# Performance work log

Measured on AMD Instinct MI355X. Metric: run time of the kernel, lower is better.

The kernel has to match this reference:

```python
import jax, jax.numpy as jnp
import numpy as np


def setup_inputs() -> dict:
    key = jax.random.key(0)
    x = jax.random.normal(key, (4096, 512), dtype=jnp.float32)
    return {"x": x}


def reference(x):
    # Pairwise Euclidean distances for all (i, j) with i > j, flattened in the
    # same order as the original nested loop: (1,0),(2,0),(2,1),(3,0),...
    n = x.shape[0]
    sq = jnp.sum(x * x, axis=1)                      # [N]
    gram = x @ x.T                                   # [N, N]
    d2 = sq[:, None] + sq[None, :] - 2.0 * gram      # [N, N] squared dists
    ii, jj = jnp.tril_indices(n, k=-1)               # row-major lower triangle
    return jnp.sqrt(jnp.maximum(d2[ii, jj], 0.0))    # [N*(N-1)/2]
```

## Files before the change

kernel.cpp:

```cpp
#include <hip/hip_runtime.h>
#include <hip/hip_bf16.h>
#include <stdint.h>

#define N 4096
#define D 512
#define TILE 128
#define BK 128
#define KITERS (D / BK)
#define NB (N / TILE)

typedef float f32x4 __attribute__((ext_vector_type(4)));
typedef int   i32x8 __attribute__((ext_vector_type(8)));
typedef int   i32x4 __attribute__((ext_vector_type(4)));

__global__ __launch_bounds__(256) void prep_kernel(const float* __restrict__ x,
                                                   unsigned char* __restrict__ xq,
                                                   float* __restrict__ sq) {
    int row  = blockIdx.x * 4 + (threadIdx.x >> 6);
    int lane = threadIdx.x & 63;
    const float* xr = x + (size_t)row * D + lane * 8;
    float4 v0 = *reinterpret_cast<const float4*>(xr);
    float4 v1 = *reinterpret_cast<const float4*>(xr + 4);

    int w0 = __builtin_amdgcn_cvt_pk_fp8_f32(v0.x, v0.y, 0, false);
    w0     = __builtin_amdgcn_cvt_pk_fp8_f32(v0.z, v0.w, w0, true);
    int w1 = __builtin_amdgcn_cvt_pk_fp8_f32(v1.x, v1.y, 0, false);
    w1     = __builtin_amdgcn_cvt_pk_fp8_f32(v1.z, v1.w, w1, true);
    reinterpret_cast<int2*>(xq + (size_t)row * D)[lane] = make_int2(w0, w1);

    float s = v0.x * v0.x + v0.y * v0.y + v0.z * v0.z + v0.w * v0.w +
              v1.x * v1.x + v1.y * v1.y + v1.z * v1.z + v1.w * v1.w;
    #pragma unroll
    for (int off = 32; off > 0; off >>= 1) s += __shfl_down(s, off);
    if (lane == 0) sq[row] = s;
}

__global__ __launch_bounds__(256, 2) void pairdist_kernel(const unsigned char* __restrict__ xq,
                                                          const float* __restrict__ sq,
                                                          float* __restrict__ out) {
    __shared__ __align__(16) unsigned char As[TILE * BK];
    __shared__ __align__(16) unsigned char Bs[TILE * BK];

    int t  = blockIdx.x;
    int bi = (int)((sqrtf(8.0f * (float)t + 1.0f) - 1.0f) * 0.5f);
    while ((bi + 1) * (bi + 2) / 2 <= t) bi++;
    while (bi * (bi + 1) / 2 > t) bi--;
    int bj = t - bi * (bi + 1) / 2;

    int tid  = threadIdx.x;
    int w    = tid >> 6;
    int lane = tid & 63;
    int quad = lane >> 4;
    int lr   = lane & 15;
    int wm   = w >> 1;
    int wn   = w & 1;

    f32x4 acc[4][4];
    #pragma unroll
    for (int mt = 0; mt < 4; mt++)
        #pragma unroll
        for (int nt = 0; nt < 4; nt++)
            acc[mt][nt] = (f32x4)0.0f;

    int srow   = lane >> 3;
    int schunk = lane & 7;
    int sw     = ((schunk ^ srow) << 4);
    const unsigned char* ga = xq + (size_t)(bi * TILE + w * 32 + srow) * D + sw;
    const unsigned char* gb = xq + (size_t)(bj * TILE + w * 32 + srow) * D + sw;
    unsigned char* la = As + w * 32 * BK;
    unsigned char* lb = Bs + w * 32 * BK;

    for (int k0 = 0; k0 < D; k0 += BK) {
        __syncthreads();
        #pragma unroll
        for (int g = 0; g < 4; g++) {
            __builtin_amdgcn_global_load_lds(
                (const __attribute__((address_space(1))) void*)(ga + k0 + (size_t)g * 8 * D),
                (__attribute__((address_space(3))) void*)(la + g * 8 * BK), 16, 0, 0);
            __builtin_amdgcn_global_load_lds(
                (const __attribute__((address_space(1))) void*)(gb + k0 + (size_t)g * 8 * D),
                (__attribute__((address_space(3))) void*)(lb + g * 8 * BK), 16, 0, 0);
        }
        __syncthreads();

        int c0 = (((2 * quad) ^ (lr & 7)) << 4);
        int c1 = c0 ^ 16;
        i32x8 af[4], bfr[4];
        #pragma unroll
        for (int mt = 0; mt < 4; mt++) {
            const unsigned char* rb = As + (wm * 64 + mt * 16 + lr) * BK;
            i32x4 lo = *reinterpret_cast<const i32x4*>(rb + c0);
            i32x4 hi = *reinterpret_cast<const i32x4*>(rb + c1);
            af[mt][0] = lo[0]; af[mt][1] = lo[1]; af[mt][2] = lo[2]; af[mt][3] = lo[3];
            af[mt][4] = hi[0]; af[mt][5] = hi[1]; af[mt][6] = hi[2]; af[mt][7] = hi[3];
        }
        #pragma unroll
        for (int nt = 0; nt < 4; nt++) {
            const unsigned char* rb = Bs + (wn * 64 + nt * 16 + lr) * BK;
            i32x4 lo = *reinterpret_cast<const i32x4*>(rb + c0);
            i32x4 hi = *reinterpret_cast<const i32x4*>(rb + c1);
            bfr[nt][0] = lo[0]; bfr[nt][1] = lo[1]; bfr[nt][2] = lo[2]; bfr[nt][3] = lo[3];
            bfr[nt][4] = hi[0]; bfr[nt][5] = hi[1]; bfr[nt][6] = hi[2]; bfr[nt][7] = hi[3];
        }

        #pragma unroll
        for (int mt = 0; mt < 4; mt++)
            #pragma unroll
            for (int nt = 0; nt < 4; nt++)
                acc[mt][nt] = __builtin_amdgcn_mfma_scale_f32_16x16x128_f8f6f4(
                    af[mt], bfr[nt], acc[mt][nt],
                    0, 0,
                    0, 0x7F7F7F7F,
                    0, 0x7F7F7F7F);
    }

    int ibase = bi * TILE + wm * 64;
    int jbase = bj * TILE + wn * 64;

    float sqi[4][4], sqj[4];
    #pragma unroll
    for (int mt = 0; mt < 4; mt++)
        #pragma unroll
        for (int tt = 0; tt < 4; tt++)
            sqi[mt][tt] = sq[ibase + mt * 16 + quad * 4 + tt];
    #pragma unroll
    for (int nt = 0; nt < 4; nt++)
        sqj[nt] = sq[jbase + nt * 16 + lr];

    if (bi != bj) {
        #pragma unroll
        for (int mt = 0; mt < 4; mt++) {
            #pragma unroll
            for (int tt = 0; tt < 4; tt++) {
                int i = ibase + mt * 16 + quad * 4 + tt;
                unsigned rowoff = (unsigned)(i * (i - 1) / 2);
                #pragma unroll
                for (int nt = 0; nt < 4; nt++) {
                    int j = jbase + nt * 16 + lr;
                    float d2 = sqi[mt][tt] + sqj[nt] - 2.0f * acc[mt][nt][tt];
                    out[rowoff + (unsigned)j] = sqrtf(fmaxf(d2, 0.0f));
                }
            }
        }
    } else {
        #pragma unroll
        for (int mt = 0; mt < 4; mt++) {
            #pragma unroll
            for (int tt = 0; tt < 4; tt++) {
                int i = ibase + mt * 16 + quad * 4 + tt;
                unsigned rowoff = (unsigned)(i * (i - 1) / 2);
                #pragma unroll
                for (int nt = 0; nt < 4; nt++) {
                    int j = jbase + nt * 16 + lr;
                    if (j < i) {
                        float d2 = sqi[mt][tt] + sqj[nt] - 2.0f * acc[mt][nt][tt];
                        out[rowoff + (unsigned)j] = sqrtf(fmaxf(d2, 0.0f));
                    }
                }
            }
        }
    }
}

extern "C" void kernel_launch(void* const* d_in, const int* in_sizes, int n_in,
                              void* d_out, int out_size, void* d_ws, size_t ws_size,
                              hipStream_t stream) {
    const float* x = (const float*)d_in[0];
    float* out = (float*)d_out;

    unsigned char* xq = (unsigned char*)d_ws;
    float* sq = (float*)((char*)d_ws + (size_t)N * D);

    prep_kernel<<<N / 4, 256, 0, stream>>>(x, xq, sq);

    int nblocks = NB * (NB + 1) / 2;
    pairdist_kernel<<<nblocks, 256, 0, stream>>>(xq, sq, out);
}
```

Before: 80.47 us.

## Load MFMA operands directly from global memory, dropping LDS staging

Removes the shared-memory tiles and the async global-to-LDS copies with their barriers. Each lane now reads its fp8 MFMA operand fragments straight from global memory (L2/L1 cached) and fully unrolls the four K iterations. This removes LDS traffic and synchronisation and frees occupancy, but every wave fetches its own copy of data that waves used to share through LDS, raising cache and global traffic.

Result: slower. 99.14 us (+23.2%).

```diff
diff --git a/kernel.cpp b/kernel.cpp
--- a/kernel.cpp
+++ b/kernel.cpp
@@ -5,8 +5,7 @@
 #define N 4096
 #define D 512
 #define TILE 128
-#define BK 128
-#define KITERS (D / BK)
+#define KITERS 4
 #define NB (N / TILE)
 
 typedef float f32x4 __attribute__((ext_vector_type(4)));
@@ -38,9 +37,6 @@
 __global__ __launch_bounds__(256, 2) void pairdist_kernel(const unsigned char* __restrict__ xq,
                                                           const float* __restrict__ sq,
                                                           float* __restrict__ out) {
-    __shared__ __align__(16) unsigned char As[TILE * BK];
-    __shared__ __align__(16) unsigned char Bs[TILE * BK];
-
     int t  = blockIdx.x;
     int bi = (int)((sqrtf(8.0f * (float)t + 1.0f) - 1.0f) * 0.5f);
     while ((bi + 1) * (bi + 2) / 2 <= t) bi++;
@@ -55,6 +51,9 @@
     int wm   = w >> 1;
     int wn   = w & 1;
 
+    int ibase = bi * TILE + wm * 64;
+    int jbase = bj * TILE + wn * 64;
+
     f32x4 acc[4][4];
     #pragma unroll
     for (int mt = 0; mt < 4; mt++)
@@ -62,43 +61,30 @@
         for (int nt = 0; nt < 4; nt++)
             acc[mt][nt] = (f32x4)0.0f;
 
-    int srow   = lane >> 3;
-    int schunk = lane & 7;
-    int sw     = ((schunk ^ srow) << 4);
-    const unsigned char* ga = xq + (size_t)(bi * TILE + w * 32 + srow) * D + sw;
-    const unsigned char* gb = xq + (size_t)(bj * TILE + w * 32 + srow) * D + sw;
-    unsigned char* la = As + w * 32 * BK;
-    unsigned char* lb = Bs + w * 32 * BK;
+    const unsigned char* pa[4];
+    const unsigned char* pb[4];
+    #pragma unroll
+    for (int mt = 0; mt < 4; mt++)
+        pa[mt] = xq + (size_t)(ibase + mt * 16 + lr) * D + quad * 32;
+    #pragma unroll
+    for (int nt = 0; nt < 4; nt++)
+        pb[nt] = xq + (size_t)(jbase + nt * 16 + lr) * D + quad * 32;
 
-    for (int k0 = 0; k0 < D; k0 += BK) {
-        __syncthreads();
-        #pragma unroll
-        for (int g = 0; g < 4; g++) {
-            __builtin_amdgcn_global_load_lds(
-                (const __attribute__((address_space(1))) void*)(ga + k0 + (size_t)g * 8 * D),
-                (__attribute__((address_space(3))) void*)(la + g * 8 * BK), 16, 0, 0);
-            __builtin_amdgcn_global_load_lds(
-                (const __attribute__((address_space(1))) void*)(gb + k0 + (size_t)g * 8 * D),
-                (__attribute__((address_space(3))) void*)(lb + g * 8 * BK), 16, 0, 0);
-        }
-        __syncthreads();
-
-        int c0 = (((2 * quad) ^ (lr & 7)) << 4);
-        int c1 = c0 ^ 16;
+    #pragma unroll
+    for (int it = 0; it < KITERS; ++it) {
+        const int k0 = it * 128;
         i32x8 af[4], bfr[4];
         #pragma unroll
         for (int mt = 0; mt < 4; mt++) {
-            const unsigned char* rb = As + (wm * 64 + mt * 16 + lr) * BK;
-            i32x4 lo = *reinterpret_cast<const i32x4*>(rb + c0);
-            i32x4 hi = *reinterpret_cast<const i32x4*>(rb + c1);
+            i32x4 lo = *reinterpret_cast<const i32x4*>(pa[mt] + k0);
+            i32x4 hi = *reinterpret_cast<const i32x4*>(pa[mt] + k0 + 16);
             af[mt][0] = lo[0]; af[mt][1] = lo[1]; af[mt][2] = lo[2]; af[mt][3] = lo[3];
             af[mt][4] = hi[0]; af[mt][5] = hi[1]; af[mt][6] = hi[2]; af[mt][7] = hi[3];
         }
         #pragma unroll
         for (int nt = 0; nt < 4; nt++) {
-            const unsigned char* rb = Bs + (wn * 64 + nt * 16 + lr) * BK;
-            i32x4 lo = *reinterpret_cast<const i32x4*>(rb + c0);
-            i32x4 hi = *reinterpret_cast<const i32x4*>(rb + c1);
+            i32x4 lo = *reinterpret_cast<const i32x4*>(pb[nt] + k0);
+            i32x4 hi = *reinterpret_cast<const i32x4*>(pb[nt] + k0 + 16);
             bfr[nt][0] = lo[0]; bfr[nt][1] = lo[1]; bfr[nt][2] = lo[2]; bfr[nt][3] = lo[3];
             bfr[nt][4] = hi[0]; bfr[nt][5] = hi[1]; bfr[nt][6] = hi[2]; bfr[nt][7] = hi[3];
         }
@@ -113,9 +99,6 @@
                     0, 0x7F7F7F7F,
                     0, 0x7F7F7F7F);
     }
-
-    int ibase = bi * TILE + wm * 64;
-    int jbase = bj * TILE + wn * 64;
 
     float sqi[4][4], sqj[4];
     #pragma unroll
```
